# Performance work log

Hardware: AMD Instinct MI355X
Metric: run time of the kernel (lower is better)

## Reference

```python
import jax, jax.numpy as jnp
import numpy as np

B, T, D = 16, 1024, 1024
H, HS = 16, 64  # num_heads, attention_head_size; H*HS == D
NEG_INF = -1e9


def setup_inputs() -> dict:
    key = jax.random.key(0)
    ks = jax.random.split(key, 6)
    s = 0.02
    x = jax.random.normal(ks[0], (B, T, D), dtype=jnp.float32)
    Wq = jax.random.normal(ks[1], (D, HS), dtype=jnp.float32) * s
    Wk = jax.random.normal(ks[2], (D, HS), dtype=jnp.float32) * s
    Wv = jax.random.normal(ks[3], (D, HS), dtype=jnp.float32) * s
    Wp = jax.random.normal(ks[4], (D, D), dtype=jnp.float32) * s
    bp = jax.random.normal(ks[5], (D,), dtype=jnp.float32) * s
    return {"x": x, "Wq": Wq, "Wk": Wk, "Wv": Wv, "Wp": Wp, "bp": bp}


def reference(x, Wq, Wk, Wv, Wp, bp):
    # Single shared Head (ModuleList([Head(...)] * num_heads) shares weights).
    q = jnp.einsum('btd,dh->bth', x, Wq)  # [B,T,HS]
    k = jnp.einsum('btd,dh->bth', x, Wk)
    v = jnp.einsum('btd,dh->bth', x, Wv)
    scale = 1.0 / jnp.sqrt(jnp.float32(HS))
    scores = jnp.einsum('bth,bsh->bts', q, k) * scale  # [B,T,T]
    causal = jnp.tril(jnp.ones((T, T), dtype=bool))
    scores = jnp.where(causal[None, :, :], scores, NEG_INF)
    attn = jax.nn.softmax(scores, axis=-1)
    head_out = jnp.einsum('bts,bsh->bth', attn, v)  # [B,T,HS]
    # Concatenate H identical head outputs along feature dim -> [B,T,D]
    out = jnp.tile(head_out, (1, 1, H))
    out = jnp.einsum('btd,de->bte', out, Wp) + bp
    return out
```

## Files before the change

### kernel.cpp

```cpp
#include <hip/hip_runtime.h>
#include <hip/hip_bf16.h>
#include <cstddef>

typedef __attribute__((ext_vector_type(8))) __bf16 bf16x8;
typedef __attribute__((ext_vector_type(4))) float f32x4;

static __device__ __forceinline__ unsigned short f2bf(float f) {
    __bf16 h = (__bf16)f;
    return __builtin_bit_cast(unsigned short, h);
}

__global__ void prep_weights(const float* __restrict__ Wq, const float* __restrict__ Wk,
                             const float* __restrict__ Wv, const float* __restrict__ Wp,
                             unsigned short* __restrict__ Wfrag,
                             unsigned short* __restrict__ WpFrag) {
    int blk = blockIdx.x;
    if (blk < 768) {
        int idx = blk * 256 + threadIdx.x;
        int CB = idx >> 14;
        int rem = idx & 16383;
        int S = rem >> 9;
        int r2 = rem & 511;
        int l = r2 >> 3, j = r2 & 7;
        int col = CB * 16 + (l & 15);
        int k = S * 32 + (l >> 4) * 8 + j;
        float v;
        if (col < 64)       v = Wq[k * 64 + col];
        else if (col < 128) v = Wk[k * 64 + (col - 64)];
        else                v = Wv[k * 64 + (col - 128)];
        Wfrag[idx] = f2bf(v);
    } else {
        int idx = (blk - 768) * 256 + threadIdx.x;
        int CB = idx >> 10;
        int rem = idx & 1023;
        int s = rem >> 9;
        int r2 = rem & 511;
        int l = r2 >> 3, j = r2 & 7;
        int col = CB * 16 + (l & 15);
        int h = s * 32 + (l >> 4) * 8 + j;
        float sum = 0.f;
#pragma unroll
        for (int j16 = 0; j16 < 16; ++j16) sum += Wp[(size_t)(j16 * 64 + h) * 1024 + col];
        WpFrag[idx] = f2bf(sum);
    }
}

__global__ __launch_bounds__(256) void qkv_gemm(const float* __restrict__ x,
                                                const unsigned short* __restrict__ Wfrag,
                                                unsigned short* __restrict__ qs,
                                                unsigned short* __restrict__ ks,
                                                unsigned short* __restrict__ vT) {
    __shared__ __align__(16) unsigned short xl[2][32 * 64];

    const int tid = threadIdx.x;
    const int lane = tid & 63;
    const int w = tid >> 6;
    const int g = lane >> 4, c = lane & 15;
    const int row0 = blockIdx.x * 32;

    const int srow = tid >> 3;
    const int scolb = (tid & 7) * 16;
    const float* xsrc = x + (size_t)(row0 + srow) * 1024 + (tid & 7) * 8;
    const int sdst = srow * 128 + (scolb ^ ((srow & 7) << 4));

    f32x4 acc[2][3];
#pragma unroll
    for (int mr = 0; mr < 2; ++mr)
#pragma unroll
        for (int cb = 0; cb < 3; ++cb) acc[mr][cb] = (f32x4){0.f, 0.f, 0.f, 0.f};

    float4 pre0[2], pre1[2];
    pre0[0] = *(const float4*)(xsrc);
    pre0[1] = *(const float4*)(xsrc + 4);
    pre1[0] = *(const float4*)(xsrc + 64);
    pre1[1] = *(const float4*)(xsrc + 68);
    {
        bf16x8 vv;
        vv[0] = (__bf16)pre0[0].x; vv[1] = (__bf16)pre0[0].y; vv[2] = (__bf16)pre0[0].z; vv[3] = (__bf16)pre0[0].w;
        vv[4] = (__bf16)pre0[1].x; vv[5] = (__bf16)pre0[1].y; vv[6] = (__bf16)pre0[1].z; vv[7] = (__bf16)pre0[1].w;
        *(bf16x8*)((char*)xl[0] + sdst) = vv;
    }
    __syncthreads();

#pragma unroll
    for (int t = 0; t < 16; ++t) {
        if (t + 2 < 16) {
            if ((t & 1) == 0) {
                pre0[0] = *(const float4*)(xsrc + (t + 2) * 64);
                pre0[1] = *(const float4*)(xsrc + (t + 2) * 64 + 4);
            } else {
                pre1[0] = *(const float4*)(xsrc + (t + 2) * 64);
                pre1[1] = *(const float4*)(xsrc + (t + 2) * 64 + 4);
            }
        }
#pragma unroll
        for (int s = 0; s < 2; ++s) {
            bf16x8 af[2];
#pragma unroll
            for (int mr = 0; mr < 2; ++mr) {
                int row = mr * 16 + c;
                af[mr] = *(const bf16x8*)((char*)xl[t & 1] + row * 128 +
                                          ((s * 64 + g * 16) ^ ((c & 7) << 4)));
            }
            int SB = t * 2 + s;
#pragma unroll
            for (int cb = 0; cb < 3; ++cb) {
                bf16x8 b = *(const bf16x8*)(Wfrag + ((size_t)((w * 3 + cb) * 32 + SB) * 512) + lane * 8);
                acc[0][cb] = __builtin_amdgcn_mfma_f32_16x16x32_bf16(af[0], b, acc[0][cb], 0, 0, 0);
                acc[1][cb] = __builtin_amdgcn_mfma_f32_16x16x32_bf16(af[1], b, acc[1][cb], 0, 0, 0);
            }
        }
        if (t < 15) {
            bf16x8 vv;
            if ((t & 1) == 0) {
                vv[0] = (__bf16)pre1[0].x; vv[1] = (__bf16)pre1[0].y; vv[2] = (__bf16)pre1[0].z; vv[3] = (__bf16)pre1[0].w;
                vv[4] = (__bf16)pre1[1].x; vv[5] = (__bf16)pre1[1].y; vv[6] = (__bf16)pre1[1].z; vv[7] = (__bf16)pre1[1].w;
                *(bf16x8*)((char*)xl[1] + sdst) = vv;
            } else {
                vv[0] = (__bf16)pre0[0].x; vv[1] = (__bf16)pre0[0].y; vv[2] = (__bf16)pre0[0].z; vv[3] = (__bf16)pre0[0].w;
                vv[4] = (__bf16)pre0[1].x; vv[5] = (__bf16)pre0[1].y; vv[6] = (__bf16)pre0[1].z; vv[7] = (__bf16)pre0[1].w;
                *(bf16x8*)((char*)xl[0] + sdst) = vv;
            }
        }
        __syncthreads();
    }

    const float QSCALE = 0.125f * 1.44269504088896340736f;
#pragma unroll
    for (int mr = 0; mr < 2; ++mr) {
#pragma unroll
        for (int cb = 0; cb < 3; ++cb) {
            int col = w * 48 + cb * 16 + c;
            int rowb = row0 + mr * 16 + g * 4;
            if (col < 64) {
#pragma unroll
                for (int r = 0; r < 4; ++r)
                    qs[(size_t)(rowb + r) * 64 + col] = f2bf(acc[mr][cb][r] * QSCALE);
            } else if (col < 128) {
#pragma unroll
                for (int r = 0; r < 4; ++r)
                    ks[(size_t)(rowb + r) * 64 + (col - 64)] = f2bf(acc[mr][cb][r]);
            } else {
                int h = col - 128;
                int b = rowb >> 10, trow = rowb & 1023;
                unsigned long long dv =
                    (unsigned long long)f2bf(acc[mr][cb][0]) |
                    ((unsigned long long)f2bf(acc[mr][cb][1]) << 16) |
                    ((unsigned long long)f2bf(acc[mr][cb][2]) << 32) |
                    ((unsigned long long)f2bf(acc[mr][cb][3]) << 48);
                *(unsigned long long*)(vT + (size_t)b * 65536 + (size_t)h * 1024 + trow) = dv;
            }
        }
    }
}

__global__ __launch_bounds__(256) void attn(const unsigned short* __restrict__ qs,
                                            const unsigned short* __restrict__ ks,
                                            const unsigned short* __restrict__ vT,
                                            unsigned short* __restrict__ ho) {
    __shared__ unsigned short Plds[4][16 * 40];
    __shared__ float oL[2][1024];
    __shared__ float pL[2][256];

    const int tid = threadIdx.x;
    const int lane = tid & 63;
    const int wid = tid >> 6;
    const int slot = wid >> 1;
    const int half = wid & 1;
    const int g = lane >> 4, c = lane & 15;

    const int tau = blockIdx.x * 2 + slot;
    const int b = tau & 15;
    const int qidx = 63 - (tau >> 4);
    const int qr0 = qidx * 16;
    const int qend = qr0 + 16;
    const int nc = (qidx >> 1) + 1;
    const int c0 = half ? (nc >> 1) : 0;
    const int c1 = half ? nc : (nc >> 1);

    const unsigned short* qbase = qs + ((size_t)b * 1024 + qr0 + c) * 64 + g * 8;
    bf16x8 aq0 = *(const bf16x8*)(qbase);
    bf16x8 aq1 = *(const bf16x8*)(qbase + 32);

    const unsigned short* kB = ks + (size_t)b * 1024 * 64;
    const unsigned short* vB = vT + (size_t)b * 64 * 1024;

    f32x4 o[4];
#pragma unroll
    for (int i = 0; i < 4; ++i) o[i] = (f32x4){0.f, 0.f, 0.f, 0.f};
    float psum[4] = {0.f, 0.f, 0.f, 0.f};
    const f32x4 zero = {0.f, 0.f, 0.f, 0.f};

    bf16x8 kc0, kc1, kc2, kc3, vc0, vc1, vc2, vc3;
    if (c0 < c1) {
        const unsigned short* kp = kB + (size_t)(c0 * 32 + c) * 64 + g * 8;
        kc0 = *(const bf16x8*)(kp);
        kc1 = *(const bf16x8*)(kp + 32);
        kc2 = *(const bf16x8*)(kp + 16 * 64);
        kc3 = *(const bf16x8*)(kp + 16 * 64 + 32);
        const unsigned short* vp = vB + (size_t)c * 1024 + c0 * 32 + g * 8;
        vc0 = *(const bf16x8*)(vp);
        vc1 = *(const bf16x8*)(vp + 16 * 1024);
        vc2 = *(const bf16x8*)(vp + 32 * 1024);
        vc3 = *(const bf16x8*)(vp + 48 * 1024);
    }

    for (int ci = c0; ci < c1; ++ci) {
        const int j0 = ci * 32;
        const bool full = (j0 + 16 < qend);
        f32x4 s0 = __builtin_amdgcn_mfma_f32_16x16x32_bf16(aq0, kc0, zero, 0, 0, 0);
        s0 = __builtin_amdgcn_mfma_f32_16x16x32_bf16(aq1, kc1, s0, 0, 0, 0);
        f32x4 s1 = zero;
        if (full) {
            s1 = __builtin_amdgcn_mfma_f32_16x16x32_bf16(aq0, kc2, zero, 0, 0, 0);
            s1 = __builtin_amdgcn_mfma_f32_16x16x32_bf16(aq1, kc3, s1, 0, 0, 0);
        }

        bf16x8 kn0, kn1, kn2, kn3, vn0, vn1, vn2, vn3;
        if (ci + 1 < c1) {
            const int jn = (ci + 1) * 32;
            const unsigned short* kp = kB + (size_t)(jn + c) * 64 + g * 8;
            kn0 = *(const bf16x8*)(kp);
            kn1 = *(const bf16x8*)(kp + 32);
            kn2 = *(const bf16x8*)(kp + 16 * 64);
            kn3 = *(const bf16x8*)(kp + 16 * 64 + 32);
            const unsigned short* vp = vB + (size_t)c * 1024 + jn + g * 8;
            vn0 = *(const bf16x8*)(vp);
            vn1 = *(const bf16x8*)(vp + 16 * 1024);
            vn2 = *(const bf16x8*)(vp + 32 * 1024);
            vn3 = *(const bf16x8*)(vp + 48 * 1024);
        }

#pragma unroll
        for (int r = 0; r < 4; ++r) {
            int t = qr0 + g * 4 + r;
            float e0 = (j0 + c > t) ? 0.f : exp2f(s0[r]);
            float e1 = (!full || j0 + 16 + c > t) ? 0.f : exp2f(s1[r]);
            psum[r] += e0 + e1;
            Plds[wid][(g * 4 + r) * 40 + c]      = f2bf(e0);
            Plds[wid][(g * 4 + r) * 40 + 16 + c] = f2bf(e1);
        }
        bf16x8 pa = *(const bf16x8*)(&Plds[wid][c * 40 + g * 8]);
        o[0] = __builtin_amdgcn_mfma_f32_16x16x32_bf16(pa, vc0, o[0], 0, 0, 0);
        o[1] = __builtin_amdgcn_mfma_f32_16x16x32_bf16(pa, vc1, o[1], 0, 0, 0);
        o[2] = __builtin_amdgcn_mfma_f32_16x16x32_bf16(pa, vc2, o[2], 0, 0, 0);
        o[3] = __builtin_amdgcn_mfma_f32_16x16x32_bf16(pa, vc3, o[3], 0, 0, 0);

        kc0 = kn0; kc1 = kn1; kc2 = kn2; kc3 = kn3;
        vc0 = vn0; vc1 = vn1; vc2 = vn2; vc3 = vn3;
    }

    if (half == 1) {
#pragma unroll
        for (int hb = 0; hb < 4; ++hb)
            *(f32x4*)&oL[slot][(hb * 64 + lane) * 4] = o[hb];
        f32x4 pv = {psum[0], psum[1], psum[2], psum[3]};
        *(f32x4*)&pL[slot][lane * 4] = pv;
    }
    __syncthreads();
    if (half == 0) {
        f32x4 pv = *(const f32x4*)&pL[slot][lane * 4];
        float inv[4];
#pragma unroll
        for (int r = 0; r < 4; ++r) {
            float ps = psum[r] + pv[r];
            ps += __shfl_xor(ps, 1);
            ps += __shfl_xor(ps, 2);
            ps += __shfl_xor(ps, 4);
            ps += __shfl_xor(ps, 8);
            inv[r] = 1.f / ps;
        }
#pragma unroll
        for (int hb = 0; hb < 4; ++hb) {
            f32x4 po = *(const f32x4*)&oL[slot][(hb * 64 + lane) * 4];
#pragma unroll
            for (int r = 0; r < 4; ++r) {
                int row = qr0 + g * 4 + r;
                ho[((size_t)b * 1024 + row) * 64 + hb * 16 + c] = f2bf((o[hb][r] + po[r]) * inv[r]);
            }
        }
    }
}

__global__ __launch_bounds__(256) void proj(const unsigned short* __restrict__ ho,
                                            const unsigned short* __restrict__ WpFrag,
                                            const float* __restrict__ bp,
                                            float* __restrict__ out) {
    __shared__ __align__(16) unsigned short hl[16 * 64];
    const int tid = threadIdx.x;
    const int lane = tid & 63;
    const int w = tid >> 6;
    const int g = lane >> 4, c = lane & 15;
    const int row0 = blockIdx.x * 16;

    if (tid < 128) {
        int row = tid >> 3;
        int colb = (tid & 7) * 16;
        bf16x8 v = *(const bf16x8*)(ho + (size_t)(row0 + row) * 64 + (tid & 7) * 8);
        *(bf16x8*)((char*)hl + row * 128 + (colb ^ ((row & 7) << 4))) = v;
    }
    __syncthreads();

    bf16x8 a0 = *(const bf16x8*)((char*)hl + c * 128 + ((g * 16) ^ ((c & 7) << 4)));
    bf16x8 a1 = *(const bf16x8*)((char*)hl + c * 128 + ((64 + g * 16) ^ ((c & 7) << 4)));
    const f32x4 zero = {0.f, 0.f, 0.f, 0.f};

#pragma unroll
    for (int cb = 0; cb < 16; ++cb) {
        int CB = w * 16 + cb;
        bf16x8 b0 = *(const bf16x8*)(WpFrag + (size_t)(CB * 2 + 0) * 512 + lane * 8);
        bf16x8 b1 = *(const bf16x8*)(WpFrag + (size_t)(CB * 2 + 1) * 512 + lane * 8);
        f32x4 acc = __builtin_amdgcn_mfma_f32_16x16x32_bf16(a0, b0, zero, 0, 0, 0);
        acc = __builtin_amdgcn_mfma_f32_16x16x32_bf16(a1, b1, acc, 0, 0, 0);
        int col = CB * 16 + c;
        float bias = bp[col];
#pragma unroll
        for (int r = 0; r < 4; ++r) {
            out[(size_t)(row0 + g * 4 + r) * 1024 + col] = acc[r] + bias;
        }
    }
}

extern "C" void kernel_launch(void* const* d_in, const int* in_sizes, int n_in,
                              void* d_out, int out_size, void* d_ws, size_t ws_size,
                              hipStream_t stream) {
    (void)in_sizes; (void)n_in; (void)out_size; (void)ws_size;
    const float* x  = (const float*)d_in[0];
    const float* Wq = (const float*)d_in[1];
    const float* Wk = (const float*)d_in[2];
    const float* Wv = (const float*)d_in[3];
    const float* Wp = (const float*)d_in[4];
    const float* bp = (const float*)d_in[5];
    float* out = (float*)d_out;

    const size_t NTOK = 16 * 1024;
    unsigned short* ws = (unsigned short*)d_ws;
    unsigned short* qs     = ws;
    unsigned short* ks     = qs + NTOK * 64;
    unsigned short* vT     = ks + NTOK * 64;
    unsigned short* ho     = vT + NTOK * 64;
    unsigned short* Wfrag  = ho + NTOK * 64;
    unsigned short* WpFrag = Wfrag + 192 * 1024;

    prep_weights<<<1024, 256, 0, stream>>>(Wq, Wk, Wv, Wp, Wfrag, WpFrag);
    qkv_gemm<<<512, 256, 0, stream>>>(x, Wfrag, qs, ks, vT);
    attn<<<512, 256, 0, stream>>>(qs, ks, vT, ho);
    proj<<<1024, 256, 0, stream>>>(ho, WpFrag, bp, out);
}
```

Baseline: 62.97 us.

## Fuse attention with output projection and shrink QKV GEMM tile to 16 rows

Merges the attention and projection kernels so each 128-thread block computes a 16-row query tile, keeps the normalized head output in shared memory, and directly runs the Wp projection and writes the final output. This removes the ho round trip through global memory and one kernel launch. The QKV GEMM now uses 16-row tiles with 128-wide K steps, which doubles the grid to 1024 blocks for better CU occupancy but halves reuse of each weight fragment. Attention blocks shrink from two query tiles to one, and each fused block does 32 projection column tiles per wave, which lengthens the per-block tail.

After: 62.08 us. No clear change (-1.4%).

```diff
diff --git a/kernel.cpp b/kernel.cpp
--- a/kernel.cpp
+++ b/kernel.cpp
@@ -50,30 +50,28 @@
                                                 unsigned short* __restrict__ qs,
                                                 unsigned short* __restrict__ ks,
                                                 unsigned short* __restrict__ vT) {
-    __shared__ __align__(16) unsigned short xl[2][32 * 64];
+    __shared__ __align__(16) unsigned short xl[2][16 * 128];
 
     const int tid = threadIdx.x;
     const int lane = tid & 63;
     const int w = tid >> 6;
     const int g = lane >> 4, c = lane & 15;
-    const int row0 = blockIdx.x * 32;
-
-    const int srow = tid >> 3;
-    const int scolb = (tid & 7) * 16;
-    const float* xsrc = x + (size_t)(row0 + srow) * 1024 + (tid & 7) * 8;
-    const int sdst = srow * 128 + (scolb ^ ((srow & 7) << 4));
-
-    f32x4 acc[2][3];
-#pragma unroll
-    for (int mr = 0; mr < 2; ++mr)
-#pragma unroll
-        for (int cb = 0; cb < 3; ++cb) acc[mr][cb] = (f32x4){0.f, 0.f, 0.f, 0.f};
+    const int row0 = blockIdx.x * 16;
+
+    const int srow = tid >> 4;
+    const int scolf = (tid & 15) * 8;
+    const float* xsrc = x + (size_t)(row0 + srow) * 1024 + scolf;
+    const int sdst = srow * 256 + ((scolf * 2) ^ ((srow & 7) << 4));
+
+    f32x4 acc[3];
+#pragma unroll
+    for (int cb = 0; cb < 3; ++cb) acc[cb] = (f32x4){0.f, 0.f, 0.f, 0.f};
 
     float4 pre0[2], pre1[2];
     pre0[0] = *(const float4*)(xsrc);
     pre0[1] = *(const float4*)(xsrc + 4);
-    pre1[0] = *(const float4*)(xsrc + 64);
-    pre1[1] = *(const float4*)(xsrc + 68);
+    pre1[0] = *(const float4*)(xsrc + 128);
+    pre1[1] = *(const float4*)(xsrc + 132);
     {
         bf16x8 vv;
         vv[0] = (__bf16)pre0[0].x; vv[1] = (__bf16)pre0[0].y; vv[2] = (__bf16)pre0[0].z; vv[3] = (__bf16)pre0[0].w;
@@ -83,34 +81,28 @@
     __syncthreads();
 
 #pragma unroll
-    for (int t = 0; t < 16; ++t) {
-        if (t + 2 < 16) {
+    for (int t = 0; t < 8; ++t) {
+        if (t + 2 < 8) {
             if ((t & 1) == 0) {
-                pre0[0] = *(const float4*)(xsrc + (t + 2) * 64);
-                pre0[1] = *(const float4*)(xsrc + (t + 2) * 64 + 4);
+                pre0[0] = *(const float4*)(xsrc + (t + 2) * 128);
+                pre0[1] = *(const float4*)(xsrc + (t + 2) * 128 + 4);
             } else {
-                pre1[0] = *(const float4*)(xsrc + (t + 2) * 64);
-                pre1[1] = *(const float4*)(xsrc + (t + 2) * 64 + 4);
+                pre1[0] = *(const float4*)(xsrc + (t + 2) * 128);
+                pre1[1] = *(const float4*)(xsrc + (t + 2) * 128 + 4);
             }
         }
 #pragma unroll
-        for (int s = 0; s < 2; ++s) {
-            bf16x8 af[2];
-#pragma unroll
-            for (int mr = 0; mr < 2; ++mr) {
-                int row = mr * 16 + c;
-                af[mr] = *(const bf16x8*)((char*)xl[t & 1] + row * 128 +
-                                          ((s * 64 + g * 16) ^ ((c & 7) << 4)));
-            }
-            int SB = t * 2 + s;
+        for (int s = 0; s < 4; ++s) {
+            bf16x8 af = *(const bf16x8*)((char*)xl[t & 1] + c * 256 +
+                                         ((s * 64 + g * 16) ^ ((c & 7) << 4)));
+            int SB = t * 4 + s;
 #pragma unroll
             for (int cb = 0; cb < 3; ++cb) {
                 bf16x8 b = *(const bf16x8*)(Wfrag + ((size_t)((w * 3 + cb) * 32 + SB) * 512) + lane * 8);
-                acc[0][cb] = __builtin_amdgcn_mfma_f32_16x16x32_bf16(af[0], b, acc[0][cb], 0, 0, 0);
-                acc[1][cb] = __builtin_amdgcn_mfma_f32_16x16x32_bf16(af[1], b, acc[1][cb], 0, 0, 0);
+                acc[cb] = __builtin_amdgcn_mfma_f32_16x16x32_bf16(af, b, acc[cb], 0, 0, 0);
             }
         }
-        if (t < 15) {
+        if (t < 7) {
             bf16x8 vv;
             if ((t & 1) == 0) {
                 vv[0] = (__bf16)pre1[0].x; vv[1] = (__bf16)pre1[0].y; vv[2] = (__bf16)pre1[0].z; vv[3] = (__bf16)pre1[0].w;
@@ -127,49 +119,47 @@
 
     const float QSCALE = 0.125f * 1.44269504088896340736f;
 #pragma unroll
-    for (int mr = 0; mr < 2; ++mr) {
-#pragma unroll
-        for (int cb = 0; cb < 3; ++cb) {
-            int col = w * 48 + cb * 16 + c;
-            int rowb = row0 + mr * 16 + g * 4;
-            if (col < 64) {
-#pragma unroll
-                for (int r = 0; r < 4; ++r)
-                    qs[(size_t)(rowb + r) * 64 + col] = f2bf(acc[mr][cb][r] * QSCALE);
-            } else if (col < 128) {
-#pragma unroll
-                for (int r = 0; r < 4; ++r)
-                    ks[(size_t)(rowb + r) * 64 + (col - 64)] = f2bf(acc[mr][cb][r]);
-            } else {
-                int h = col - 128;
-                int b = rowb >> 10, trow = rowb & 1023;
-                unsigned long long dv =
-                    (unsigned long long)f2bf(acc[mr][cb][0]) |
-                    ((unsigned long long)f2bf(acc[mr][cb][1]) << 16) |
-                    ((unsigned long long)f2bf(acc[mr][cb][2]) << 32) |
-                    ((unsigned long long)f2bf(acc[mr][cb][3]) << 48);
-                *(unsigned long long*)(vT + (size_t)b * 65536 + (size_t)h * 1024 + trow) = dv;
-            }
-        }
-    }
-}
-
-__global__ __launch_bounds__(256) void attn(const unsigned short* __restrict__ qs,
-                                            const unsigned short* __restrict__ ks,
-                                            const unsigned short* __restrict__ vT,
-                                            unsigned short* __restrict__ ho) {
-    __shared__ unsigned short Plds[4][16 * 40];
-    __shared__ float oL[2][1024];
-    __shared__ float pL[2][256];
+    for (int cb = 0; cb < 3; ++cb) {
+        int col = w * 48 + cb * 16 + c;
+        int rowb = row0 + g * 4;
+        if (col < 64) {
+#pragma unroll
+            for (int r = 0; r < 4; ++r)
+                qs[(size_t)(rowb + r) * 64 + col] = f2bf(acc[cb][r] * QSCALE);
+        } else if (col < 128) {
+#pragma unroll
+            for (int r = 0; r < 4; ++r)
+                ks[(size_t)(rowb + r) * 64 + (col - 64)] = f2bf(acc[cb][r]);
+        } else {
+            int h = col - 128;
+            int b = rowb >> 10, trow = rowb & 1023;
+            unsigned long long dv =
+                (unsigned long long)f2bf(acc[cb][0]) |
+                ((unsigned long long)f2bf(acc[cb][1]) << 16) |
+                ((unsigned long long)f2bf(acc[cb][2]) << 32) |
+                ((unsigned long long)f2bf(acc[cb][3]) << 48);
+            *(unsigned long long*)(vT + (size_t)b * 65536 + (size_t)h * 1024 + trow) = dv;
+        }
+    }
+}
+
+__global__ __launch_bounds__(128) void attn_proj(const unsigned short* __restrict__ qs,
+                                                 const unsigned short* __restrict__ ks,
+                                                 const unsigned short* __restrict__ vT,
+                                                 const unsigned short* __restrict__ WpFrag,
+                                                 const float* __restrict__ bp,
+                                                 float* __restrict__ out) {
+    __shared__ unsigned short Plds[2][16 * 40];
+    __shared__ float oL[1024];
+    __shared__ float pL[256];
+    __shared__ __align__(16) unsigned short hl[16 * 64];
 
     const int tid = threadIdx.x;
     const int lane = tid & 63;
-    const int wid = tid >> 6;
-    const int slot = wid >> 1;
-    const int half = wid & 1;
+    const int half = tid >> 6;
     const int g = lane >> 4, c = lane & 15;
 
-    const int tau = blockIdx.x * 2 + slot;
+    const int tau = blockIdx.x;
     const int b = tau & 15;
     const int qidx = 63 - (tau >> 4);
     const int qr0 = qidx * 16;
@@ -237,10 +227,10 @@
             float e0 = (j0 + c > t) ? 0.f : exp2f(s0[r]);
             float e1 = (!full || j0 + 16 + c > t) ? 0.f : exp2f(s1[r]);
             psum[r] += e0 + e1;
-            Plds[wid][(g * 4 + r) * 40 + c]      = f2bf(e0);
-            Plds[wid][(g * 4 + r) * 40 + 16 + c] = f2bf(e1);
-        }
-        bf16x8 pa = *(const bf16x8*)(&Plds[wid][c * 40 + g * 8]);
+            Plds[half][(g * 4 + r) * 40 + c]      = f2bf(e0);
+            Plds[half][(g * 4 + r) * 40 + 16 + c] = f2bf(e1);
+        }
+        bf16x8 pa = *(const bf16x8*)(&Plds[half][c * 40 + g * 8]);
         o[0] = __builtin_amdgcn_mfma_f32_16x16x32_bf16(pa, vc0, o[0], 0, 0, 0);
         o[1] = __builtin_amdgcn_mfma_f32_16x16x32_bf16(pa, vc1, o[1], 0, 0, 0);
         o[2] = __builtin_amdgcn_mfma_f32_16x16x32_bf16(pa, vc2, o[2], 0, 0, 0);
@@ -253,13 +243,13 @@
     if (half == 1) {
 #pragma unroll
         for (int hb = 0; hb < 4; ++hb)
-            *(f32x4*)&oL[slot][(hb * 64 + lane) * 4] = o[hb];
+            *(f32x4*)&oL[(hb * 64 + lane) * 4] = o[hb];
         f32x4 pv = {psum[0], psum[1], psum[2], psum[3]};
-        *(f32x4*)&pL[slot][lane * 4] = pv;
+        *(f32x4*)&pL[lane * 4] = pv;
     }
     __syncthreads();
     if (half == 0) {
-        f32x4 pv = *(const f32x4*)&pL[slot][lane * 4];
+        f32x4 pv = *(const f32x4*)&pL[lane * 4];
         float inv[4];
 #pragma unroll
         for (int r = 0; r < 4; ++r) {
@@ -272,42 +262,24 @@
         }
 #pragma unroll
         for (int hb = 0; hb < 4; ++hb) {
-            f32x4 po = *(const f32x4*)&oL[slot][(hb * 64 + lane) * 4];
+            f32x4 po = *(const f32x4*)&oL[(hb * 64 + lane) * 4];
 #pragma unroll
             for (int r = 0; r < 4; ++r) {
-                int row = qr0 + g * 4 + r;
-                ho[((size_t)b * 1024 + row) * 64 + hb * 16 + c] = f2bf((o[hb][r] + po[r]) * inv[r]);
+                int row = g * 4 + r;
+                int colb = (hb * 16 + c) * 2;
+                *(unsigned short*)((char*)hl + row * 128 + (colb ^ ((row & 7) << 4))) =
+                    f2bf((o[hb][r] + po[r]) * inv[r]);
             }
         }
-    }
-}
-
-__global__ __launch_bounds__(256) void proj(const unsigned short* __restrict__ ho,
-                                            const unsigned short* __restrict__ WpFrag,
-                                            const float* __restrict__ bp,
-                                            float* __restrict__ out) {
-    __shared__ __align__(16) unsigned short hl[16 * 64];
-    const int tid = threadIdx.x;
-    const int lane = tid & 63;
-    const int w = tid >> 6;
-    const int g = lane >> 4, c = lane & 15;
-    const int row0 = blockIdx.x * 16;
-
-    if (tid < 128) {
-        int row = tid >> 3;
-        int colb = (tid & 7) * 16;
-        bf16x8 v = *(const bf16x8*)(ho + (size_t)(row0 + row) * 64 + (tid & 7) * 8);
-        *(bf16x8*)((char*)hl + row * 128 + (colb ^ ((row & 7) << 4))) = v;
     }
     __syncthreads();
 
     bf16x8 a0 = *(const bf16x8*)((char*)hl + c * 128 + ((g * 16) ^ ((c & 7) << 4)));
     bf16x8 a1 = *(const bf16x8*)((char*)hl + c * 128 + ((64 + g * 16) ^ ((c & 7) << 4)));
-    const f32x4 zero = {0.f, 0.f, 0.f, 0.f};
-
-#pragma unroll
-    for (int cb = 0; cb < 16; ++cb) {
-        int CB = w * 16 + cb;
+    const size_t obase = ((size_t)b * 1024 + qr0) * 1024;
+#pragma unroll
+    for (int cb = 0; cb < 32; ++cb) {
+        int CB = half * 32 + cb;
         bf16x8 b0 = *(const bf16x8*)(WpFrag + (size_t)(CB * 2 + 0) * 512 + lane * 8);
         bf16x8 b1 = *(const bf16x8*)(WpFrag + (size_t)(CB * 2 + 1) * 512 + lane * 8);
         f32x4 acc = __builtin_amdgcn_mfma_f32_16x16x32_bf16(a0, b0, zero, 0, 0, 0);
@@ -316,7 +288,7 @@
         float bias = bp[col];
 #pragma unroll
         for (int r = 0; r < 4; ++r) {
-            out[(size_t)(row0 + g * 4 + r) * 1024 + col] = acc[r] + bias;
+            out[obase + (size_t)(g * 4 + r) * 1024 + col] = acc[r] + bias;
         }
     }
 }
@@ -338,12 +310,10 @@
     unsigned short* qs     = ws;
     unsigned short* ks     = qs + NTOK * 64;
     unsigned short* vT     = ks + NTOK * 64;
-    unsigned short* ho     = vT + NTOK * 64;
-    unsigned short* Wfrag  = ho + NTOK * 64;
+    unsigned short* Wfrag  = vT + NTOK * 64;
     unsigned short* WpFrag = Wfrag + 192 * 1024;
 
     prep_weights<<<1024, 256, 0, stream>>>(Wq, Wk, Wv, Wp, Wfrag, WpFrag);
-    qkv_gemm<<<512, 256, 0, stream>>>(x, Wfrag, qs, ks, vT);
-    attn<<<512, 256, 0, stream>>>(qs, ks, vT, ho);
-    proj<<<1024, 256, 0, stream>>>(ho, WpFrag, bp, out);
-}
+    qkv_gemm<<<1024, 256, 0, stream>>>(x, Wfrag, qs, ks, vT);
+    attn_proj<<<1024, 128, 0, stream>>>(qs, ks, vT, WpFrag, bp, out);
+}
```
